# Performance work log

Hardware: AMD Instinct MI355X
Metric: run time of the kernel (lower is better)

Reference implementation:

```python
import jax, jax.numpy as jnp
import numpy as np
import math

B, L, E, H = 512, 200, 64, 4
D = E // H
NEG = jnp.float32(-(2.0 ** 32) + 1.0)


def setup_inputs() -> dict:
    key = jax.random.key(0)
    ks = jax.random.split(key, 12)
    inp = jax.random.normal(ks[0], (B, L, E), dtype=jnp.float32)
    # realistic variable-length histories: mask[b, t] = t < len_b, len_b in [1, L]
    lens = jax.random.randint(ks[1], (B, 1), 1, L + 1)
    mask = jnp.arange(L)[None, :] < lens  # [B, L] bool
    s = 1.0 / math.sqrt(E)
    pos_enc = jax.random.normal(ks[2], (1, L, E), dtype=jnp.float32)
    Wk = jax.random.uniform(ks[3], (E, E), jnp.float32, -s, s)
    bk = jnp.zeros((E,), jnp.float32)
    Wv = jax.random.uniform(ks[4], (E, E), jnp.float32, -s, s)
    bv = jnp.zeros((E,), jnp.float32)
    Wq = jax.random.uniform(ks[5], (E, E), jnp.float32, -s, s)
    bq = jnp.zeros((E,), jnp.float32)
    Wf = jax.random.uniform(ks[6], (E, E), jnp.float32, -s, s)
    bf = jnp.zeros((E,), jnp.float32)
    return {"input": inp, "mask": mask, "pos_enc": pos_enc,
            "Wk": Wk, "bk": bk, "Wv": Wv, "bv": bv,
            "Wq": Wq, "bq": bq, "Wf": Wf, "bf": bf}


def reference(input, mask, pos_enc, Wk, bk, Wv, bv, Wq, bq, Wf, bf):
    x = input + pos_enc  # [B, L, E]
    # project and split heads: [B, H, L, D]
    def split(t):
        return t.reshape(B, L, H, D).transpose(0, 2, 1, 3)
    k = split(x @ Wk.T + bk)
    v = split(x @ Wv.T + bv)
    q = split(x @ Wq.T + bq) / math.sqrt(D)
    scores = jnp.einsum('bhqd,bhkd->bhqk', q, k)  # [B, H, L, L]
    # key_mask in torch code broadcasts over dim 3 (mask on the QUERY axis),
    # query_mask is its transpose (mask on the KEY axis). Combined: both must be valid.
    both = mask[:, None, :, None] & mask[:, None, None, :]  # [B, 1, L, L]
    scores = jnp.where(both, scores, NEG)
    attn = jax.nn.softmax(scores, axis=-1)
    # dropout is identity at inference; omitted deterministically
    out = jnp.einsum('bhqk,bhkd->bhqd', attn, v)
    out = out.transpose(0, 2, 1, 3).reshape(B, L, E)
    out = out @ Wf.T + bf
    fm = mask.astype(jnp.float32)[:, :, None]  # [B, L, 1]
    lens = jnp.sum(fm, axis=1)  # [B, 1]
    pooled = jnp.sum(out * fm, axis=1) / (lens + 1e-8)  # [B, E]
    return pooled
```

## Files before the change

### kernel.cpp

```cpp
#include <hip/hip_runtime.h>
#include <hip/hip_fp16.h>
#include <math.h>

#define Bn 512
#define Ln 200
#define En 64
#define Hn 4
#define Dn 16
#define KS3 18
#define VS3 200
#define QSC 0.36067376022224085f

typedef _Float16 __f16;
typedef __fp16 fp16x2 __attribute__((ext_vector_type(2)));
typedef __f16 f16x4 __attribute__((ext_vector_type(4)));
typedef __f16 f16x8 __attribute__((ext_vector_type(8)));
typedef float f32x4 __attribute__((ext_vector_type(4)));

#if __has_builtin(__builtin_amdgcn_exp2f)
__device__ __forceinline__ float fexp2(float x) { return __builtin_amdgcn_exp2f(x); }
#else
__device__ __forceinline__ float fexp2(float x) { return exp2f(x); }
#endif

__device__ __forceinline__ f16x8 pack8s(float4 a, float4 b, float4 pa, float4 pb) {
    f16x8 r;
    r[0] = (__f16)(a.x + pa.x); r[1] = (__f16)(a.y + pa.y);
    r[2] = (__f16)(a.z + pa.z); r[3] = (__f16)(a.w + pa.w);
    r[4] = (__f16)(b.x + pb.x); r[5] = (__f16)(b.y + pb.y);
    r[6] = (__f16)(b.z + pb.z); r[7] = (__f16)(b.w + pb.w);
    return r;
}
__device__ __forceinline__ f16x8 pack8(float4 a, float4 b) {
    f16x8 r;
    r[0] = (__f16)a.x; r[1] = (__f16)a.y; r[2] = (__f16)a.z; r[3] = (__f16)a.w;
    r[4] = (__f16)b.x; r[5] = (__f16)b.y; r[6] = (__f16)b.z; r[7] = (__f16)b.w;
    return r;
}

__device__ __forceinline__ f16x4 pack4rtz(float e0, float e1, float e2, float e3) {
    const fp16x2 lo = __builtin_amdgcn_cvt_pkrtz(e0, e1);
    const fp16x2 hi = __builtin_amdgcn_cvt_pkrtz(e2, e3);
    f16x4 r;
    r[0] = (__f16)lo[0]; r[1] = (__f16)lo[1];
    r[2] = (__f16)hi[0]; r[3] = (__f16)hi[1];
    return r;
}

template<int NI>
__device__ __forceinline__ void attn_core(
    const __f16* __restrict__ Kh_, const __f16* __restrict__ Qh_, const __f16* __restrict__ Vt_,
    int qt0, int klo, int khi, int nt, int len, int quad, int ln16,
    f32x4 (&o2)[4], f32x4 (&lacc)[4])
{
    const f16x4 ones = {(__f16)1.f, (__f16)1.f, (__f16)1.f, (__f16)1.f};
    f16x4 qf[NI];
    #pragma unroll
    for (int i = 0; i < NI; ++i) {
        int qr = min((qt0 + i) * 16 + ln16, Ln - 1);
        qf[i] = *(const f16x4*)(Qh_ + qr * KS3 + quad * 4);
    }
    const bool needmask = (khi == nt);
    const int kfull = khi - (needmask ? 1 : 0);

    f16x4 kf = *(const f16x4*)(Kh_ + min(klo * 16 + ln16, Ln - 1) * KS3 + quad * 4);
    f16x4 vf = *(const f16x4*)(Vt_ + ln16 * VS3 + min(klo * 16 + quad * 4, Ln - 4));

    for (int kt = klo; kt < kfull; ++kt) {
        const int krn = min((kt + 1) * 16 + ln16, Ln - 1);
        const int vcn = min((kt + 1) * 16 + quad * 4, Ln - 4);
        const f16x4 kfn = *(const f16x4*)(Kh_ + krn * KS3 + quad * 4);
        const f16x4 vfn = *(const f16x4*)(Vt_ + ln16 * VS3 + vcn);
        f32x4 s[NI];
        __builtin_amdgcn_s_setprio(1);
        #pragma unroll
        for (int i = 0; i < NI; ++i)
            s[i] = __builtin_amdgcn_mfma_f32_16x16x16f16(kf, qf[i], (f32x4){0,0,0,0}, 0, 0, 0);
        __builtin_amdgcn_s_setprio(0);
        f16x4 pf[NI];
        #pragma unroll
        for (int i = 0; i < NI; ++i) {
            pf[i] = pack4rtz(fexp2(fminf(s[i][0], 14.5f)),
                             fexp2(fminf(s[i][1], 14.5f)),
                             fexp2(fminf(s[i][2], 14.5f)),
                             fexp2(fminf(s[i][3], 14.5f)));
        }
        __builtin_amdgcn_s_setprio(1);
        #pragma unroll
        for (int i = 0; i < NI; ++i) {
            o2[i]   = __builtin_amdgcn_mfma_f32_16x16x16f16(vf,   pf[i], o2[i],   0, 0, 0);
            lacc[i] = __builtin_amdgcn_mfma_f32_16x16x16f16(ones, pf[i], lacc[i], 0, 0, 0);
        }
        __builtin_amdgcn_s_setprio(0);
        kf = kfn; vf = vfn;
    }
    if (needmask) {
        const int kbase = (nt - 1) * 16 + quad * 4;
        f32x4 s[NI];
        __builtin_amdgcn_s_setprio(1);
        #pragma unroll
        for (int i = 0; i < NI; ++i)
            s[i] = __builtin_amdgcn_mfma_f32_16x16x16f16(kf, qf[i], (f32x4){0,0,0,0}, 0, 0, 0);
        __builtin_amdgcn_s_setprio(0);
        f16x4 pf[NI];
        #pragma unroll
        for (int i = 0; i < NI; ++i) {
            float e[4];
            #pragma unroll
            for (int j = 0; j < 4; ++j) {
                const bool kok = (kbase + j) < len;
                e[j] = kok ? fexp2(fminf(s[i][j], 14.5f)) : 0.f;
            }
            pf[i] = pack4rtz(e[0], e[1], e[2], e[3]);
        }
        __builtin_amdgcn_s_setprio(1);
        #pragma unroll
        for (int i = 0; i < NI; ++i) {
            o2[i]   = __builtin_amdgcn_mfma_f32_16x16x16f16(vf,   pf[i], o2[i],   0, 0, 0);
            lacc[i] = __builtin_amdgcn_mfma_f32_16x16x16f16(ones, pf[i], lacc[i], 0, 0, 0);
        }
        __builtin_amdgcn_s_setprio(0);
    }
}

__global__ __launch_bounds__(256, 4) void fused_kernel(
    const float* __restrict__ input, const int* __restrict__ mask,
    const float* __restrict__ pos_enc,
    const float* __restrict__ Wk, const float* __restrict__ bk,
    const float* __restrict__ Wv, const float* __restrict__ bv,
    const float* __restrict__ Wq, const float* __restrict__ bq,
    const float* __restrict__ Wf, const float* __restrict__ bf_,
    float* __restrict__ out)
{
    __shared__ __align__(16) __f16 Kh[Ln * KS3];
    __shared__ __align__(16) __f16 Qh[Ln * KS3];
    __shared__ __align__(16) __f16 Vt[16 * VS3];
    __shared__ float lred[4][4][16];
    __shared__ float red[4][16];
    __shared__ float ph[16];
    __shared__ int cnt_red[4];

    const int tid  = threadIdx.x;
    const int b    = blockIdx.x >> 2, h = blockIdx.x & 3;
    const int wave = tid >> 6, lane = tid & 63;
    const int quad = lane >> 4, ln16 = lane & 15;

    const int mv = (tid < Ln) ? mask[b * Ln + tid] : 0;

    f16x8 bfr[3][2];
    #pragma unroll
    for (int m = 0; m < 3; ++m) {
        const float* W = (m == 0) ? Wk : (m == 1) ? Wv : Wq;
        #pragma unroll
        for (int ks = 0; ks < 2; ++ks) {
            const float4* wp = (const float4*)(W + (size_t)(h * 16 + ln16) * 64) + (ks * 8 + quad * 2);
            bfr[m][ks] = pack8(wp[0], wp[1]);
        }
    }
    const int cg = h * 16 + ln16;
    const float bkv = bk[cg], bvv = bv[cg], bqv = bq[cg];

    int c = (mv != 0) ? 1 : 0;
    #pragma unroll
    for (int off = 32; off; off >>= 1) c += __shfl_down(c, off, 64);
    if (lane == 0) cnt_red[wave] = c;
    __syncthreads();
    const int len = cnt_red[0] + cnt_red[1] + cnt_red[2] + cnt_red[3];
    const int nt = (len + 15) >> 4;

    const float4* in4 = (const float4*)(input + (size_t)b * Ln * En);
    const float4* pe4 = (const float4*)pos_enc;

    for (int rt = wave; rt < nt; rt += 4) {
        const int R = rt * 16 + ln16;
        const bool rok = (R < Ln);
        f16x8 af[2];
        #pragma unroll
        for (int ks = 0; ks < 2; ++ks) {
            float4 xa = {0,0,0,0}, xb = {0,0,0,0}, pa = {0,0,0,0}, pb = {0,0,0,0};
            if (rok) {
                const int o4 = R * 16 + ks * 8 + quad * 2;
                xa = in4[o4]; xb = in4[o4 + 1];
                pa = pe4[o4]; pb = pe4[o4 + 1];
            }
            af[ks] = pack8s(xa, xb, pa, pb);
        }
        f32x4 acc[3];
        #pragma unroll
        for (int m = 0; m < 3; ++m) acc[m] = (f32x4){0,0,0,0};
        #pragma unroll
        for (int ks = 0; ks < 2; ++ks)
            #pragma unroll
            for (int m = 0; m < 3; ++m)
                acc[m] = __builtin_amdgcn_mfma_f32_16x16x32_f16(af[ks], bfr[m][ks], acc[m], 0, 0, 0);

        #pragma unroll
        for (int j = 0; j < 4; ++j) {
            const int t = rt * 16 + quad * 4 + j;
            if (t < Ln) {
                Kh[t * KS3 + ln16] = (__f16)(acc[0][j] + bkv);
                Qh[t * KS3 + ln16] = (__f16)((acc[2][j] + bqv) * QSC);
            }
        }
        const int vc0 = rt * 16 + quad * 4;
        if (vc0 < Ln) {
            f16x4 vp;
            #pragma unroll
            for (int j = 0; j < 4; ++j) vp[j] = (__f16)(acc[1][j] + bvv);
            *(f16x4*)(Vt + ln16 * VS3 + vc0) = vp;
        }
    }
    __syncthreads();

    const int nquad = (nt + 3) >> 2;
    int g, kh, nkh;
    if (nquad >= 3)      { g = wave;     kh = 0;         nkh = 1; }
    else if (nquad == 2) { g = wave & 1; kh = wave >> 1; nkh = 2; }
    else                 { g = 0;        kh = wave;      nkh = 4; }
    const bool active = (g < nquad);
    const int nktp = (nt + nkh - 1) / nkh;
    const int klo = kh * nktp;
    const int khi = min(klo + nktp, nt);
    const int qt0 = 4 * g;

    f32x4 o2[4], lacc[4];
    #pragma unroll
    for (int i = 0; i < 4; ++i) { o2[i] = (f32x4){0,0,0,0}; lacc[i] = (f32x4){0,0,0,0}; }

    if (active && klo < khi) {
        const int ni = __builtin_amdgcn_readfirstlane(min(4, nt - qt0));
        switch (ni) {
            case 1:  attn_core<1>(Kh, Qh, Vt, qt0, klo, khi, nt, len, quad, ln16, o2, lacc); break;
            case 2:  attn_core<2>(Kh, Qh, Vt, qt0, klo, khi, nt, len, quad, ln16, o2, lacc); break;
            case 3:  attn_core<3>(Kh, Qh, Vt, qt0, klo, khi, nt, len, quad, ln16, o2, lacc); break;
            default: attn_core<4>(Kh, Qh, Vt, qt0, klo, khi, nt, len, quad, ln16, o2, lacc); break;
        }
    }

    float l[4];
    #pragma unroll
    for (int i = 0; i < 4; ++i) l[i] = lacc[i][0];

    if (nkh > 1) {
        if (lane < 16) {
            #pragma unroll
            for (int i = 0; i < 4; ++i) lred[wave][i][lane] = l[i];
        }
        __syncthreads();
        #pragma unroll
        for (int i = 0; i < 4; ++i) {
            if (nkh == 2) l[i] = lred[g][i][ln16] + lred[g + 2][i][ln16];
            else          l[i] = lred[0][i][ln16] + lred[1][i][ln16]
                               + lred[2][i][ln16] + lred[3][i][ln16];
        }
    }

    f32x4 pool = {0.f, 0.f, 0.f, 0.f};
    if (active) {
        #pragma unroll
        for (int i = 0; i < 4; ++i) {
            const float rs = ((qt0 + i) * 16 + ln16 < len) ? 1.f / l[i] : 0.f;
            #pragma unroll
            for (int j = 0; j < 4; ++j) pool[j] = fmaf(o2[i][j], rs, pool[j]);
        }
    }

    #pragma unroll
    for (int j = 0; j < 4; ++j) {
        #pragma unroll
        for (int off = 1; off < 16; off <<= 1) pool[j] += __shfl_xor(pool[j], off, 64);
    }
    if (ln16 == 0) {
        #pragma unroll
        for (int j = 0; j < 4; ++j) red[wave][quad * 4 + j] = pool[j];
    }
    __syncthreads();
    if (tid < 16)
        ph[tid] = (red[0][tid] + red[1][tid] + red[2][tid] + red[3][tid]) / ((float)len + 1e-8f);
    __syncthreads();

    if (tid < 64) {
        const int e = tid;
        const float* wr = Wf + (size_t)e * 64 + h * 16;
        float a = (h == 0) ? bf_[e] : 0.f;
        #pragma unroll
        for (int i = 0; i < 16; ++i) a = fmaf(wr[i], ph[i], a);
        atomicAdd(out + b * En + e, a);
    }
}

extern "C" void kernel_launch(void* const* d_in, const int* in_sizes, int n_in,
                              void* d_out, int out_size, void* d_ws, size_t ws_size,
                              hipStream_t stream) {
    const float* input   = (const float*)d_in[0];
    const int*   mask    = (const int*)  d_in[1];
    const float* pos_enc = (const float*)d_in[2];
    const float* Wk      = (const float*)d_in[3];
    const float* bk      = (const float*)d_in[4];
    const float* Wv      = (const float*)d_in[5];
    const float* bv      = (const float*)d_in[6];
    const float* Wq      = (const float*)d_in[7];
    const float* bq      = (const float*)d_in[8];
    const float* Wf      = (const float*)d_in[9];
    const float* bf      = (const float*)d_in[10];

    float* out = (float*)d_out;
    hipMemsetAsync(out, 0, (size_t)Bn * En * sizeof(float), stream);

    fused_kernel<<<Bn * Hn, 256, 0, stream>>>(input, mask, pos_enc,
                                              Wk, bk, Wv, bv, Wq, bq, Wf, bf, out);
}
```

Before: 124.3 us.

## Prefetch input rows across loop iterations, swizzle block mapping, drop setprio

Each wave's first input row tile is now loaded before the mask reduction and barrier, and the next tile is prefetched in registers while the current one is processed, hiding global-load latency behind the projection MFMAs. Block indices are remapped so consecutive blocks spread across the 8 XCD groups. The s_setprio hints around the attention MFMAs are removed. The cost is higher register pressure, a possibly wasted first load when the sequence is short, and changed wave scheduling.

```diff
diff --git a/kernel.cpp b/kernel.cpp
--- a/kernel.cpp
+++ b/kernel.cpp
@@ -72,11 +72,9 @@
         const f16x4 kfn = *(const f16x4*)(Kh_ + krn * KS3 + quad * 4);
         const f16x4 vfn = *(const f16x4*)(Vt_ + ln16 * VS3 + vcn);
         f32x4 s[NI];
-        __builtin_amdgcn_s_setprio(1);
         #pragma unroll
         for (int i = 0; i < NI; ++i)
             s[i] = __builtin_amdgcn_mfma_f32_16x16x16f16(kf, qf[i], (f32x4){0,0,0,0}, 0, 0, 0);
-        __builtin_amdgcn_s_setprio(0);
         f16x4 pf[NI];
         #pragma unroll
         for (int i = 0; i < NI; ++i) {
@@ -85,23 +83,19 @@
                              fexp2(fminf(s[i][2], 14.5f)),
                              fexp2(fminf(s[i][3], 14.5f)));
         }
-        __builtin_amdgcn_s_setprio(1);
         #pragma unroll
         for (int i = 0; i < NI; ++i) {
             o2[i]   = __builtin_amdgcn_mfma_f32_16x16x16f16(vf,   pf[i], o2[i],   0, 0, 0);
             lacc[i] = __builtin_amdgcn_mfma_f32_16x16x16f16(ones, pf[i], lacc[i], 0, 0, 0);
         }
-        __builtin_amdgcn_s_setprio(0);
         kf = kfn; vf = vfn;
     }
     if (needmask) {
         const int kbase = (nt - 1) * 16 + quad * 4;
         f32x4 s[NI];
-        __builtin_amdgcn_s_setprio(1);
         #pragma unroll
         for (int i = 0; i < NI; ++i)
             s[i] = __builtin_amdgcn_mfma_f32_16x16x16f16(kf, qf[i], (f32x4){0,0,0,0}, 0, 0, 0);
-        __builtin_amdgcn_s_setprio(0);
         f16x4 pf[NI];
         #pragma unroll
         for (int i = 0; i < NI; ++i) {
@@ -113,13 +107,11 @@
             }
             pf[i] = pack4rtz(e[0], e[1], e[2], e[3]);
         }
-        __builtin_amdgcn_s_setprio(1);
         #pragma unroll
         for (int i = 0; i < NI; ++i) {
             o2[i]   = __builtin_amdgcn_mfma_f32_16x16x16f16(vf,   pf[i], o2[i],   0, 0, 0);
             lacc[i] = __builtin_amdgcn_mfma_f32_16x16x16f16(ones, pf[i], lacc[i], 0, 0, 0);
         }
-        __builtin_amdgcn_s_setprio(0);
     }
 }
 
@@ -141,9 +133,20 @@
     __shared__ int cnt_red[4];
 
     const int tid  = threadIdx.x;
-    const int b    = blockIdx.x >> 2, h = blockIdx.x & 3;
+    const int lin  = ((blockIdx.x & 7) << 8) | (blockIdx.x >> 3);
+    const int b    = lin >> 2, h = lin & 3;
     const int wave = tid >> 6, lane = tid & 63;
     const int quad = lane >> 4, ln16 = lane & 15;
+
+    const float4* in4 = (const float4*)(input + (size_t)b * Ln * En);
+    const float4* pe4 = (const float4*)pos_enc;
+
+    float4 px0, px1, px2, px3;
+    {
+        const int o4 = (wave * 16 + ln16) * 16 + quad * 2;
+        px0 = in4[o4];     px1 = in4[o4 + 1];
+        px2 = in4[o4 + 8]; px3 = in4[o4 + 9];
+    }
 
     const int mv = (tid < Ln) ? mask[b * Ln + tid] : 0;
 
@@ -168,31 +171,36 @@
     const int len = cnt_red[0] + cnt_red[1] + cnt_red[2] + cnt_red[3];
     const int nt = (len + 15) >> 4;
 
-    const float4* in4 = (const float4*)(input + (size_t)b * Ln * En);
-    const float4* pe4 = (const float4*)pos_enc;
-
     for (int rt = wave; rt < nt; rt += 4) {
         const int R = rt * 16 + ln16;
         const bool rok = (R < Ln);
-        f16x8 af[2];
-        #pragma unroll
-        for (int ks = 0; ks < 2; ++ks) {
-            float4 xa = {0,0,0,0}, xb = {0,0,0,0}, pa = {0,0,0,0}, pb = {0,0,0,0};
-            if (rok) {
-                const int o4 = R * 16 + ks * 8 + quad * 2;
-                xa = in4[o4]; xb = in4[o4 + 1];
-                pa = pe4[o4]; pb = pe4[o4 + 1];
-            }
-            af[ks] = pack8s(xa, xb, pa, pb);
-        }
+        const int o4 = R * 16 + quad * 2;
+
+        const int rtn = rt + 4;
+        const int Rn = rtn * 16 + ln16;
+        float4 pxn0 = {0,0,0,0}, pxn1 = {0,0,0,0}, pxn2 = {0,0,0,0}, pxn3 = {0,0,0,0};
+        if (rtn < nt && Rn < Ln) {
+            const int o4n = Rn * 16 + quad * 2;
+            pxn0 = in4[o4n];     pxn1 = in4[o4n + 1];
+            pxn2 = in4[o4n + 8]; pxn3 = in4[o4n + 9];
+        }
+        float4 pp0 = {0,0,0,0}, pp1 = {0,0,0,0}, pp2 = {0,0,0,0}, pp3 = {0,0,0,0};
+        if (rok) {
+            pp0 = pe4[o4];     pp1 = pe4[o4 + 1];
+            pp2 = pe4[o4 + 8]; pp3 = pe4[o4 + 9];
+        }
+        f16x8 af0 = pack8s(px0, px1, pp0, pp1);
+        f16x8 af1 = pack8s(px2, px3, pp2, pp3);
+
         f32x4 acc[3];
         #pragma unroll
         for (int m = 0; m < 3; ++m) acc[m] = (f32x4){0,0,0,0};
         #pragma unroll
-        for (int ks = 0; ks < 2; ++ks)
-            #pragma unroll
-            for (int m = 0; m < 3; ++m)
-                acc[m] = __builtin_amdgcn_mfma_f32_16x16x32_f16(af[ks], bfr[m][ks], acc[m], 0, 0, 0);
+        for (int m = 0; m < 3; ++m)
+            acc[m] = __builtin_amdgcn_mfma_f32_16x16x32_f16(af0, bfr[m][0], acc[m], 0, 0, 0);
+        #pragma unroll
+        for (int m = 0; m < 3; ++m)
+            acc[m] = __builtin_amdgcn_mfma_f32_16x16x32_f16(af1, bfr[m][1], acc[m], 0, 0, 0);
 
         #pragma unroll
         for (int j = 0; j < 4; ++j) {
@@ -209,6 +217,7 @@
             for (int j = 0; j < 4; ++j) vp[j] = (__f16)(acc[1][j] + bvv);
             *(f16x4*)(Vt + ln16 * VS3 + vc0) = vp;
         }
+        px0 = pxn0; px1 = pxn1; px2 = pxn2; px3 = pxn3;
     }
     __syncthreads();
 
```

After: 122.0 us. About the same (-1.9%).
